# Kernel optimization log

Measured on AMD Instinct MI355X. Metric: run time of the kernel, lower is better.

## Reference

```python
import jax, jax.numpy as jnp
import numpy as np

VOCAB = 32000
HID = 1024
CUTOFFS = [0, 10000, 20000, 32000]
N_CLUSTERS = 2
DIV = 4
PROJ_DIMS = [HID // DIV**i for i in range(N_CLUSTERS + 1)]  # [1024, 256, 64]
# Faithful to source quirk: n_vocabs = cutoffs[i] + cutoffs[i+1]
LOGIT_DIMS = [CUTOFFS[i] + CUTOFFS[i + 1] for i in range(N_CLUSTERS + 1)]  # [10000, 30000, 52000]


def setup_inputs() -> dict:
    key = jax.random.key(0)
    ks = jax.random.split(key, 16)
    N = 2048
    inp = {
        "x": jax.random.normal(ks[0], (N, HID), dtype=jnp.float32),
        "y": jax.random.randint(ks[1], (N,), 0, VOCAB, dtype=jnp.int64),
    }
    s = 0.02
    # projections: Linear(hidden, proj_dims[i], bias=False); stored as [in, out]
    inp["Wp0"] = jax.random.normal(ks[2], (HID, PROJ_DIMS[0]), dtype=jnp.float32) * s
    inp["Wp1"] = jax.random.normal(ks[3], (HID, PROJ_DIMS[1]), dtype=jnp.float32) * s
    inp["Wp2"] = jax.random.normal(ks[4], (HID, PROJ_DIMS[2]), dtype=jnp.float32) * s
    # logits: Linear(proj_dims[i], LOGIT_DIMS[i]) with bias
    inp["Wl0"] = jax.random.normal(ks[5], (PROJ_DIMS[0], LOGIT_DIMS[0]), dtype=jnp.float32) * s
    inp["bl0"] = jnp.zeros((LOGIT_DIMS[0],), dtype=jnp.float32)
    inp["Wl1"] = jax.random.normal(ks[6], (PROJ_DIMS[1], LOGIT_DIMS[1]), dtype=jnp.float32) * s
    inp["bl1"] = jnp.zeros((LOGIT_DIMS[1],), dtype=jnp.float32)
    inp["Wl2"] = jax.random.normal(ks[7], (PROJ_DIMS[2], LOGIT_DIMS[2]), dtype=jnp.float32) * s
    inp["bl2"] = jnp.zeros((LOGIT_DIMS[2],), dtype=jnp.float32)
    # cluster_logit: Linear(hidden, n_clusters)
    inp["Wc"] = jax.random.normal(ks[8], (HID, N_CLUSTERS), dtype=jnp.float32) * s
    inp["bc"] = jnp.zeros((N_CLUSTERS,), dtype=jnp.float32)
    return inp


def reference(x, y, Wp0, Wp1, Wp2, Wl0, bl0, Wl1, bl1, Wl2, bl2, Wc, bc):
    # head: project (dim-preserving here) then head-vocab logits + cluster logits
    head_proj = x @ Wp0                                   # [N, 1024]
    head_logit = jnp.concatenate(
        [head_proj @ Wl0 + bl0, head_proj @ Wc + bc], axis=1
    )                                                     # [N, 10000 + 2]
    head_lp = jax.nn.log_softmax(head_logit, axis=1)

    nll = jnp.zeros(y.shape, dtype=x.dtype)

    # cluster 0: targets in [0, cutoffs[1])
    m0 = (y >= CUTOFFS[0]) & (y < CUTOFFS[1])
    t0 = jnp.clip(y - CUTOFFS[0], 0, head_lp.shape[1] - 1)
    lp0 = jnp.take_along_axis(head_lp, t0[:, None], axis=1)[:, 0]
    nll = jnp.where(m0, -lp0, nll)

    # tail clusters: small projection GEMM + log_softmax + gather, combined via masks
    tails = [(Wp1, Wl1, bl1), (Wp2, Wl2, bl2)]
    for i, (Wp, Wl, bl) in enumerate(tails, start=1):
        l, r = CUTOFFS[i], CUTOFFS[i + 1]
        mask = (y >= l) & (y < r)
        t = jnp.clip(y - l, 0, Wl.shape[1] - 1)
        tail_lp = jax.nn.log_softmax((x @ Wp) @ Wl + bl, axis=1)  # [N, LOGIT_DIMS[i]]
        # faithful to source: head column -i (reversed cluster order quirk)
        lp = head_lp[:, -i] + jnp.take_along_axis(tail_lp, t[:, None], axis=1)[:, 0]
        nll = jnp.where(mask, -lp, nll)

    return nll
```

## Files before the change

kernel.cpp:

```cpp
#include <hip/hip_runtime.h>
#include <math.h>

#define HID 1024
#define NROWS 2048

typedef __attribute__((ext_vector_type(8))) short short8;
typedef __attribute__((ext_vector_type(4))) short short4_t;
typedef __attribute__((ext_vector_type(4))) float f32x4;

__device__ __forceinline__ short f2bf(float f) {
  union { float f; unsigned u; } v; v.f = f;
  unsigned r = v.u + 0x7fffu + ((v.u >> 16) & 1u);
  return (short)(r >> 16);
}
__device__ __forceinline__ float bf2f(short s) {
  union { unsigned u; float f; } v; v.u = ((unsigned)(unsigned short)s) << 16;
  return v.f;
}
__device__ __forceinline__ float wave_sum(float a) {
#pragma unroll
  for (int off = 32; off; off >>= 1) a += __shfl_xor(a, off, 64);
  return a;
}

__global__ __launch_bounds__(256) void prep(
    const float* __restrict__ x, const int* __restrict__ y,
    const float* __restrict__ Wp0, const float* __restrict__ Wp1,
    const float* __restrict__ Wp2, const float* __restrict__ Wl0,
    const float* __restrict__ Wl1, const float* __restrict__ Wl2,
    short* __restrict__ xb,
    int* __restrict__ counts, int* __restrict__ slot_of_row,
    int* __restrict__ rows1, int* __restrict__ rows2,
    short* __restrict__ T0, short* __restrict__ T1, short* __restrict__ T2,
    short* __restrict__ T3, short* __restrict__ T4, short* __restrict__ T5) {
  const int tid = threadIdx.x;
  int b = blockIdx.x;
  if (b == 0) {
    __shared__ int c1s, c2s;
    if (tid == 0) { c1s = 0; c2s = 0; }
    __syncthreads();
    for (int r = tid; r < NROWS; r += 256) {
      const int yy = y[r];
      if (yy >= 20000) {
        const int s = atomicAdd(&c2s, 1);
        slot_of_row[r] = s; rows2[s] = r;
      } else if (yy >= 10000) {
        const int s = atomicAdd(&c1s, 1);
        slot_of_row[r] = s; rows1[s] = r;
      } else {
        slot_of_row[r] = -1;
      }
    }
    __syncthreads();
    if (tid == 0) { counts[0] = NROWS; counts[1] = c1s; counts[2] = c2s; }
    return;
  }
  if (b <= 2048) {
    const int i = ((b - 1) * 256 + tid) * 4;
    short4_t o;
    o.x = f2bf(x[i + 0]); o.y = f2bf(x[i + 1]);
    o.z = f2bf(x[i + 2]); o.w = f2bf(x[i + 3]);
    *(short4_t*)&xb[i] = o;
    return;
  }
  b -= 2049;
  const float* W; short* BT; int K, N, Npad, tn;
  if (b < 1024)                { W = Wp0; BT = T0; K = 1024; N = 1024;  Npad = 1024;  tn = 32;   }
  else if ((b -= 1024) < 256)  { W = Wp1; BT = T1; K = 1024; N = 256;   Npad = 256;   tn = 8;    }
  else if ((b -= 256) < 128)   { W = Wp2; BT = T2; K = 1024; N = 64;    Npad = 128;   tn = 4;    }
  else if ((b -= 128) < 10240) { W = Wl0; BT = T3; K = 1024; N = 10000; Npad = 10240; tn = 320;  }
  else if ((b -= 10240) < 7552){ W = Wl1; BT = T4; K = 256;  N = 30000; Npad = 30208; tn = 944;  }
  else { b -= 7552;              W = Wl2; BT = T5; K = 64;   N = 52000; Npad = 52224; tn = 1632; }

  __shared__ float T[32][33];
  const int n0 = (b % tn) * 32, k0 = (b / tn) * 32;
  const int r = tid >> 3, c = (tid & 7) * 4;
  float v0 = 0.f, v1 = 0.f, v2 = 0.f, v3 = 0.f;
  const float* p = &W[(size_t)(k0 + r) * N];
  if (n0 + c + 3 < N) {
    v0 = p[n0 + c]; v1 = p[n0 + c + 1]; v2 = p[n0 + c + 2]; v3 = p[n0 + c + 3];
  } else {
    if (n0 + c + 0 < N) v0 = p[n0 + c + 0];
    if (n0 + c + 1 < N) v1 = p[n0 + c + 1];
    if (n0 + c + 2 < N) v2 = p[n0 + c + 2];
  }
  T[r][c] = v0; T[r][c + 1] = v1; T[r][c + 2] = v2; T[r][c + 3] = v3;
  __syncthreads();
  const int nl = tid >> 3, kl = (tid & 7) * 4;
  const int n = n0 + nl;
  if (n < Npad) {
    short4_t o;
    o.x = (n < N) ? f2bf(T[kl + 0][nl]) : (short)0;
    o.y = (n < N) ? f2bf(T[kl + 1][nl]) : (short)0;
    o.z = (n < N) ? f2bf(T[kl + 2][nl]) : (short)0;
    o.w = (n < N) ? f2bf(T[kl + 3][nl]) : (short)0;
    *(short4_t*)&BT[(size_t)n * K + k0 + kl] = o;
  }
}

#define GLOAD_LDS(g, l)                                                      \
  __builtin_amdgcn_global_load_lds(                                          \
      (const __attribute__((address_space(1))) void*)(g),                    \
      (__attribute__((address_space(3))) void*)(l), 16, 0, 0)

#define BARR do { asm volatile("" ::: "memory");                             \
                  __builtin_amdgcn_s_barrier();                              \
                  asm volatile("" ::: "memory"); } while (0)

#define VMW(n) asm volatile("s_waitcnt vmcnt(" #n ")" ::: "memory")

__device__ __forceinline__ void stage_half(const short* __restrict__ src,
                                           size_t row0, int kOff, short* dst,
                                           int stride, int w, int rsub, int kc) {
  const short* g0 = src + (row0 + (size_t)(w * 8 + rsub)) * (size_t)stride
                    + kOff + kc * 8;
  GLOAD_LDS(g0, dst + w * 512);
  GLOAD_LDS(g0 + (size_t)64 * stride, dst + 4096 + w * 512);
}

#define RD_A8(dst, base) do {                                                \
  _Pragma("unroll") for (int mt = 0; mt < 4; ++mt)                           \
  _Pragma("unroll") for (int kk = 0; kk < 2; ++kk)                           \
    dst[mt * 2 + kk] = *(const short8*)((base) +                             \
        (pm * 64 + mt * 16 + ln) * 64 + (((kk * 4 + quad) ^ l7) << 3));      \
} while (0)

#define RD_B4(dst, base) do {                                                \
  _Pragma("unroll") for (int nt = 0; nt < 2; ++nt)                           \
  _Pragma("unroll") for (int kk = 0; kk < 2; ++kk)                           \
    dst[nt * 2 + kk] = *(const short8*)((base) +                             \
        (pn * 32 + nt * 16 + ln) * 64 + (((kk * 4 + quad) ^ l7) << 3));      \
} while (0)

#define MFMA16(ACC, ar, br) do {                                             \
  __builtin_amdgcn_s_setprio(1);                                             \
  _Pragma("unroll") for (int mt = 0; mt < 4; ++mt)                           \
  _Pragma("unroll") for (int nt = 0; nt < 2; ++nt)                           \
  _Pragma("unroll") for (int kk = 0; kk < 2; ++kk)                           \
    ACC[mt][nt] = __builtin_amdgcn_mfma_f32_16x16x32_bf16(                   \
        ar[mt * 2 + kk], br[nt * 2 + kk], ACC[mt][nt], 0, 0, 0);             \
  __builtin_amdgcn_s_setprio(0);                                             \
} while (0)

__device__ __forceinline__ void gemm256(
    const short* __restrict__ A, const short* __restrict__ BT,
    int K, int NT, size_t rowA0, size_t rowB0, short* lds,
    f32x4 acc[2][2][4][2], int w, int lane) {
  const int quad = lane >> 4, ln = lane & 15, l7 = lane & 7;
  const int pm = w >> 2, pn = w & 3;
  const int rsub = lane >> 3, kc = (lane & 7) ^ rsub;
  short* const Abase = lds;
  short* const Bbase = lds + 32768;

  stage_half(A,  rowA0,       0, Abase,        K, w, rsub, kc);
  stage_half(BT, rowB0,       0, Bbase,        K, w, rsub, kc);
  stage_half(BT, rowB0 + 128, 0, Bbase + 8192, K, w, rsub, kc);
  stage_half(A,  rowA0 + 128, 0, Abase + 8192, K, w, rsub, kc);

  for (int u = 0; u < NT; ++u) {
    const int c = u & 1;
    const short* Ah = Abase + c * 16384;
    const short* Bh = Bbase + c * 16384;
    short* const An = Abase + (c ^ 1) * 16384;
    short* const Bn = Bbase + (c ^ 1) * 16384;
    const int k1 = (u + 1) << 6;
    const bool more = (u < NT - 1);
    short8 aq0[8], aq1[8], bq0[4], bq1[4];
    VMW(4);
    BARR;
    RD_A8(aq0, Ah);
    RD_B4(bq0, Bh);
    if (more) stage_half(A, rowA0, k1, An, K, w, rsub, kc);
    MFMA16(acc[0][0], aq0, bq0);
    if (more) { VMW(4); } else { VMW(2); }
    BARR;
    RD_B4(bq1, Bh + 8192);
    if (more) stage_half(BT, rowB0, k1, Bn, K, w, rsub, kc);
    MFMA16(acc[0][1], aq0, bq1);
    if (more) { VMW(4); } else { VMW(0); }
    BARR;
    RD_A8(aq1, Ah + 8192);
    if (more) stage_half(BT, rowB0 + 128, k1, Bn + 8192, K, w, rsub, kc);
    MFMA16(acc[1][1], aq1, bq1);
    BARR;
    if (more) stage_half(A, rowA0 + 128, k1, An + 8192, K, w, rsub, kc);
    MFMA16(acc[1][0], aq1, bq0);
  }
}


__device__ __forceinline__ void exp_epilogue(
    f32x4 acc[2][2][4][2], const float* __restrict__ bias,
    float* __restrict__ ps, size_t c0, int Ncols, int nsplit, int r0,
    short* lds, int tid, int w, int lane) {
  const int quad = lane >> 4, ln = lane & 15;
  const int pm = w >> 2, pn = w & 3;
  float bv[2][2];
#pragma unroll
  for (int qb = 0; qb < 2; ++qb)
#pragma unroll
    for (int nt = 0; nt < 2; ++nt) {
      const size_t cg = c0 + qb * 128 + pn * 32 + nt * 16 + ln;
      bv[qb][nt] = (cg < (size_t)Ncols) ? bias[cg] : -1.0e30f;
    }
  float* const psF = (float*)lds;
  BARR;
#pragma unroll
  for (int qa = 0; qa < 2; ++qa)
#pragma unroll
    for (int qb = 0; qb < 2; ++qb)
#pragma unroll
      for (int mt = 0; mt < 4; ++mt)
#pragma unroll
        for (int r = 0; r < 4; ++r) {
          float s = __expf(acc[qa][qb][mt][0][r] + bv[qb][0]) +
                    __expf(acc[qa][qb][mt][1][r] + bv[qb][1]);
#pragma unroll
          for (int off = 1; off < 16; off <<= 1) s += __shfl_xor(s, off, 64);
          if (ln == 0)
            psF[(pn * 2 + qb) * 256 + qa * 128 + pm * 64 + mt * 16 + quad * 4 + r] = s;
        }
  BARR;
  {
    const int qb = tid >> 8, row = tid & 255;
    const int cs = (int)(c0 >> 7) + qb;
    if (cs < nsplit)
      ps[(size_t)(r0 + row) * nsplit + cs] =
          psF[(0 * 2 + qb) * 256 + row] + psF[(1 * 2 + qb) * 256 + row] +
          psF[(2 * 2 + qb) * 256 + row] + psF[(3 * 2 + qb) * 256 + row];
  }
}

__device__ __forceinline__ void mfma_mainloop(const short* aB[4], const short* bB[4],
                                              short* As, short* Bs,
                                              f32x4 acc[4][4],
                                              int K, int w, int lane) {
  const int quad = lane >> 4, ln = lane & 15;
  const int wm = w >> 1, wn = w & 1;
  const int l7 = ln & 7;
  for (int kt = 0; kt < K; kt += 64) {
#pragma unroll
    for (int i = 0; i < 4; ++i) {
      const int row = w * 32 + i * 8;
      __builtin_amdgcn_global_load_lds(
          (const __attribute__((address_space(1))) void*)(aB[i] + kt),
          (__attribute__((address_space(3))) void*)(As + row * 64), 16, 0, 0);
      __builtin_amdgcn_global_load_lds(
          (const __attribute__((address_space(1))) void*)(bB[i] + kt),
          (__attribute__((address_space(3))) void*)(Bs + row * 64), 16, 0, 0);
    }
    __syncthreads();
#pragma unroll
    for (int ks = 0; ks < 2; ++ks) {
      const int kcs = ks * 4 + quad;
      short8 af[4], bfr[4];
#pragma unroll
      for (int mt = 0; mt < 4; ++mt) {
        const int row = wm * 64 + mt * 16 + ln;
        af[mt] = *(const short8*)(As + ((row * 8 + (kcs ^ l7)) << 3));
      }
#pragma unroll
      for (int nt = 0; nt < 4; ++nt) {
        const int rowb = wn * 64 + nt * 16 + ln;
        bfr[nt] = *(const short8*)(Bs + ((rowb * 8 + (kcs ^ l7)) << 3));
      }
#pragma unroll
      for (int mt = 0; mt < 4; ++mt)
#pragma unroll
        for (int nt = 0; nt < 4; ++nt)
          acc[mt][nt] = __builtin_amdgcn_mfma_f32_16x16x32_bf16(
              af[mt], bfr[nt], acc[mt][nt], 0, 0, 0);
    }
    __syncthreads();
  }
}

__global__ __launch_bounds__(256) void proj_all(
    const short* __restrict__ xb,
    const short* __restrict__ WpT0, const short* __restrict__ WpT1,
    const short* __restrict__ WpT2,
    short* __restrict__ P0b, short* __restrict__ P1c, short* __restrict__ P2c,
    const int* __restrict__ rows1, const int* __restrict__ rows2,
    const int* __restrict__ counts) {
  int b = blockIdx.x;
  const short* BT; short* C; int N, r0, c0, cnt;
  const int* rowlist = nullptr;
  if (b < 128) {
    BT = WpT0; C = P0b; N = 1024;
    c0 = (b & 7) * 128; r0 = (b >> 3) * 128; cnt = NROWS;
  } else if (b < 160) {
    b -= 128; BT = WpT1; C = P1c; N = 256;
    c0 = (b & 1) * 128; r0 = (b >> 1) * 128; rowlist = rows1; cnt = counts[1];
  } else {
    b -= 160; BT = WpT2; C = P2c; N = 64;
    c0 = 0; r0 = b * 128; rowlist = rows2; cnt = counts[2];
  }
  if (r0 >= cnt) return;

  __shared__ short As[128 * 64];
  __shared__ short Bs[128 * 64];
  const int tid = threadIdx.x;
  const int w = tid >> 6, lane = tid & 63;
  const int quad = lane >> 4, ln = lane & 15;
  const int wm = w >> 1, wn = w & 1;
  const int rsub = lane >> 3;
  const int kc = (lane & 7) ^ rsub;
  const int K = 1024;

  const short* aB[4]; const short* bB[4];
#pragma unroll
  for (int i = 0; i < 4; ++i) {
    const int sl = r0 + w * 32 + i * 8 + rsub;
    const int ar = rowlist ? rowlist[sl < cnt ? sl : cnt - 1] : sl;
    aB[i] = xb + (size_t)ar * K + kc * 8;
    bB[i] = BT + (size_t)(c0 + w * 32 + i * 8 + rsub) * K + kc * 8;
  }

  f32x4 acc[4][4];
  const f32x4 zero = {0.f, 0.f, 0.f, 0.f};
#pragma unroll
  for (int i = 0; i < 4; ++i)
#pragma unroll
    for (int j = 0; j < 4; ++j) acc[i][j] = zero;
  mfma_mainloop(aB, bB, As, Bs, acc, K, w, lane);
#pragma unroll
  for (int mt = 0; mt < 4; ++mt)
#pragma unroll
    for (int r = 0; r < 4; ++r) {
      const int grow = r0 + wm * 64 + mt * 16 + quad * 4 + r;
#pragma unroll
      for (int nt = 0; nt < 4; ++nt) {
        const int cg = c0 + wn * 64 + nt * 16 + ln;
        if (cg < N) C[(size_t)grow * N + cg] = f2bf(acc[mt][nt][r]);
      }
    }
}

__global__ __launch_bounds__(512, 2) void logit_fused(
    const short* __restrict__ P0b, const short* __restrict__ WlT0,
    const float* __restrict__ bl0, float* __restrict__ psh,
    const short* __restrict__ P1c, const short* __restrict__ WlT1,
    const float* __restrict__ bl1, float* __restrict__ ps1,
    const short* __restrict__ P2c, const short* __restrict__ WlT2,
    const float* __restrict__ bl2, float* __restrict__ ps2,
    const int* __restrict__ counts) {
  __shared__ short lds[65536];
  const int tid = threadIdx.x;
  const int w = tid >> 6, lane = tid & 63;
  const int b = blockIdx.x;

  const short* A; const short* BT; const float* bias; float* ps;
  int K, NT, Ncols, nsplit, r0; size_t c0;
  if (b < 320) {
    const int xcd = b & 7, j = b >> 3;
    const int cb = xcd * 5 + j % 5, rb = j / 5;
    r0 = rb * 256; c0 = (size_t)cb * 256;
    A = P0b; BT = WlT0; bias = bl0; ps = psh;
    K = 1024; NT = 16; Ncols = 10000; nsplit = 79;
  } else if (b < 1264) {
    const int b1 = b - 320;
    const int rb = b1 / 118, cb = b1 % 118;
    r0 = rb * 256;
    if (r0 >= counts[1]) return;
    c0 = (size_t)cb * 256;
    A = P1c; BT = WlT1; bias = bl1; ps = ps1;
    K = 256; NT = 4; Ncols = 30000; nsplit = 235;
  } else {
    const int b2 = b - 1264;
    const int rb = b2 / 204, cb = b2 % 204;
    r0 = rb * 256;
    if (r0 >= counts[2]) return;
    c0 = (size_t)cb * 256;
    A = P2c; BT = WlT2; bias = bl2; ps = ps2;
    K = 64; NT = 1; Ncols = 52000; nsplit = 407;
  }

  f32x4 acc[2][2][4][2];
  const f32x4 zero = {0.f, 0.f, 0.f, 0.f};
#pragma unroll
  for (int qa = 0; qa < 2; ++qa)
#pragma unroll
    for (int qb = 0; qb < 2; ++qb)
#pragma unroll
      for (int mt = 0; mt < 4; ++mt)
#pragma unroll
        for (int nt = 0; nt < 2; ++nt) acc[qa][qb][mt][nt] = zero;

  gemm256(A, BT, K, NT, (size_t)r0, c0, lds, acc, w, lane);
  exp_epilogue(acc, bias, ps, c0, Ncols, nsplit, r0, lds, tid, w, lane);
}

__global__ __launch_bounds__(256) void finalize(
    const short* __restrict__ P0b, const short* __restrict__ P1c,
    const short* __restrict__ P2c,
    const short* __restrict__ WlT0, const float* __restrict__ bl0,
    const short* __restrict__ WlT1, const float* __restrict__ bl1,
    const short* __restrict__ WlT2, const float* __restrict__ bl2,
    const float* __restrict__ Wc, const float* __restrict__ bc,
    const int* __restrict__ y, const int* __restrict__ slot_of_row,
    const float* __restrict__ psh, const float* __restrict__ ps1,
    const float* __restrict__ ps2, float* __restrict__ out) {
  const int lane = threadIdx.x & 63;
  const int row = blockIdx.x * 4 + (threadIdx.x >> 6);

  float a0 = 0.f, a1 = 0.f;
  for (int k = lane; k < HID; k += 64) {
    const float p = bf2f(P0b[(size_t)row * HID + k]);
    a0 += p * Wc[2 * k];
    a1 += p * Wc[2 * k + 1];
  }
  a0 = wave_sum(a0);
  a1 = wave_sum(a1);
  const float cl0 = a0 + bc[0], cl1 = a1 + bc[1];

  float S = 0.f;
  for (int i = lane; i < 79; i += 64) S += psh[(size_t)row * 79 + i];
  S = wave_sum(S) + __expf(cl0) + __expf(cl1);
  const float lse = logf(S);

  const int yy = y[row];
  float nll;
  if (yy < 10000) {
    const short* pr = P0b + (size_t)row * 1024;
    const short* wr = WlT0 + (size_t)yy * 1024;
    float a = 0.f;
    for (int kk = lane * 4; kk < 1024; kk += 256) {
      const short4_t p = *(const short4_t*)(pr + kk);
      const short4_t wv = *(const short4_t*)(wr + kk);
      a += bf2f(p.x) * bf2f(wv.x) + bf2f(p.y) * bf2f(wv.y)
         + bf2f(p.z) * bf2f(wv.z) + bf2f(p.w) * bf2f(wv.w);
    }
    a = wave_sum(a);
    nll = -((a + bl0[yy]) - lse);
  } else if (yy < 20000) {
    const int t = yy - 10000;
    const int slot = slot_of_row[row];
    float S1 = 0.f;
    for (int i = lane; i < 235; i += 64) S1 += ps1[(size_t)slot * 235 + i];
    S1 = wave_sum(S1);
    const short* pr = P1c + (size_t)slot * 256;
    const short* wr = WlT1 + (size_t)t * 256;
    const int kk = lane * 4;
    const short4_t p = *(const short4_t*)(pr + kk);
    const short4_t wv = *(const short4_t*)(wr + kk);
    float a = bf2f(p.x) * bf2f(wv.x) + bf2f(p.y) * bf2f(wv.y)
            + bf2f(p.z) * bf2f(wv.z) + bf2f(p.w) * bf2f(wv.w);
    a = wave_sum(a);
    nll = -((cl1 - lse) + ((a + bl1[t]) - logf(S1)));
  } else {
    const int t = yy - 20000;
    const int slot = slot_of_row[row];
    float S2 = 0.f;
    for (int i = lane; i < 407; i += 64) S2 += ps2[(size_t)slot * 407 + i];
    S2 = wave_sum(S2);
    float a = 0.f;
    if (lane < 16) {
      const short* pr = P2c + (size_t)slot * 64;
      const short* wr = WlT2 + (size_t)t * 64;
      const int kk = lane * 4;
      const short4_t p = *(const short4_t*)(pr + kk);
      const short4_t wv = *(const short4_t*)(wr + kk);
      a = bf2f(p.x) * bf2f(wv.x) + bf2f(p.y) * bf2f(wv.y)
        + bf2f(p.z) * bf2f(wv.z) + bf2f(p.w) * bf2f(wv.w);
    }
    a = wave_sum(a);
    nll = -((cl0 - lse) + ((a + bl2[t]) - logf(S2)));
  }
  if (lane == 0) out[row] = nll;
}

extern "C" void kernel_launch(void* const* d_in, const int* in_sizes, int n_in,
                              void* d_out, int out_size, void* d_ws, size_t ws_size,
                              hipStream_t stream) {
  const float* x   = (const float*)d_in[0];
  const int*   y   = (const int*)d_in[1];
  const float* Wp0 = (const float*)d_in[2];
  const float* Wp1 = (const float*)d_in[3];
  const float* Wp2 = (const float*)d_in[4];
  const float* Wl0 = (const float*)d_in[5];
  const float* bl0 = (const float*)d_in[6];
  const float* Wl1 = (const float*)d_in[7];
  const float* bl1 = (const float*)d_in[8];
  const float* Wl2 = (const float*)d_in[9];
  const float* bl2 = (const float*)d_in[10];
  const float* Wc  = (const float*)d_in[11];
  const float* bc  = (const float*)d_in[12];
  float* out = (float*)d_out;

  float* fws = (float*)d_ws;
  float* psh = fws; fws += (size_t)NROWS * 79;
  float* ps1 = fws; fws += (size_t)NROWS * 235;
  float* ps2 = fws; fws += (size_t)NROWS * 407;
  int* iws = (int*)fws;
  int* counts      = iws; iws += 4;
  int* slot_of_row = iws; iws += NROWS;
  int* rows1       = iws; iws += NROWS;
  int* rows2       = iws; iws += NROWS;
  short* sp = (short*)iws;
  short* xb   = sp; sp += (size_t)NROWS * 1024;
  short* P0b  = sp; sp += (size_t)NROWS * 1024;
  short* P1c  = sp; sp += (size_t)NROWS * 256;
  short* P2c  = sp; sp += (size_t)NROWS * 64;
  short* WpT0 = sp; sp += (size_t)1024 * 1024;
  short* WpT1 = sp; sp += (size_t)256 * 1024;
  short* WpT2 = sp; sp += (size_t)128 * 1024;
  short* WlT0 = sp; sp += (size_t)10240 * 1024;
  short* WlT1 = sp; sp += (size_t)30208 * 256;
  short* WlT2 = sp; sp += (size_t)52224 * 64;

  dim3 blk(256);
  prep<<<dim3(24513), blk, 0, stream>>>(x, y, Wp0, Wp1, Wp2, Wl0, Wl1, Wl2,
                                        xb, counts, slot_of_row, rows1, rows2,
                                        WpT0, WpT1, WpT2, WlT0, WlT1, WlT2);
  proj_all<<<dim3(176), blk, 0, stream>>>(xb, WpT0, WpT1, WpT2, P0b, P1c, P2c,
                                          rows1, rows2, counts);
  logit_fused<<<dim3(2896), dim3(512), 0, stream>>>(
      P0b, WlT0, bl0, psh, P1c, WlT1, bl1, ps1, P2c, WlT2, bl2, ps2, counts);
  finalize<<<dim3(NROWS / 4), blk, 0, stream>>>(
      P0b, P1c, P2c, WlT0, bl0, WlT1, bl1, WlT2, bl2, Wc, bc, y, slot_of_row,
      psh, ps1, ps2, out);
}
```

Before: 318.3 us.

## Widen prep transpose tiles and restructure logit GEMM into 8-phase pipeline

The prep kernel now handles 64x64 transpose tiles with float4 loads and short8 stores, and converts x in 4096-element chunks per block, which cuts the block count about fourfold. The logit GEMM mainloop becomes an explicit 8-phase schedule. It prefetches two K-steps up front, adds barriers and lgkmcnt waits around each MFMA group, and takes a separate single-K-step path. The aim is cheaper weight conversion and better overlap of global-to-LDS loads with MFMA. The extra barriers could add synchronisation overhead in the GEMM.

```diff
diff --git a/kernel.cpp b/kernel.cpp
--- a/kernel.cpp
+++ b/kernel.cpp
@@ -55,46 +55,59 @@
     if (tid == 0) { counts[0] = NROWS; counts[1] = c1s; counts[2] = c2s; }
     return;
   }
-  if (b <= 2048) {
-    const int i = ((b - 1) * 256 + tid) * 4;
-    short4_t o;
-    o.x = f2bf(x[i + 0]); o.y = f2bf(x[i + 1]);
-    o.z = f2bf(x[i + 2]); o.w = f2bf(x[i + 3]);
-    *(short4_t*)&xb[i] = o;
+  if (b <= 512) {
+    const int base = (b - 1) * 4096;
+#pragma unroll
+    for (int j = 0; j < 4; ++j) {
+      const int i = base + j * 1024 + tid * 4;
+      const float4 v = *(const float4*)&x[i];
+      short4_t o;
+      o.x = f2bf(v.x); o.y = f2bf(v.y); o.z = f2bf(v.z); o.w = f2bf(v.w);
+      *(short4_t*)&xb[i] = o;
+    }
     return;
   }
-  b -= 2049;
+  b -= 513;
   const float* W; short* BT; int K, N, Npad, tn;
-  if (b < 1024)                { W = Wp0; BT = T0; K = 1024; N = 1024;  Npad = 1024;  tn = 32;   }
-  else if ((b -= 1024) < 256)  { W = Wp1; BT = T1; K = 1024; N = 256;   Npad = 256;   tn = 8;    }
-  else if ((b -= 256) < 128)   { W = Wp2; BT = T2; K = 1024; N = 64;    Npad = 128;   tn = 4;    }
-  else if ((b -= 128) < 10240) { W = Wl0; BT = T3; K = 1024; N = 10000; Npad = 10240; tn = 320;  }
-  else if ((b -= 10240) < 7552){ W = Wl1; BT = T4; K = 256;  N = 30000; Npad = 30208; tn = 944;  }
-  else { b -= 7552;              W = Wl2; BT = T5; K = 64;   N = 52000; Npad = 52224; tn = 1632; }
-
-  __shared__ float T[32][33];
-  const int n0 = (b % tn) * 32, k0 = (b / tn) * 32;
-  const int r = tid >> 3, c = (tid & 7) * 4;
-  float v0 = 0.f, v1 = 0.f, v2 = 0.f, v3 = 0.f;
-  const float* p = &W[(size_t)(k0 + r) * N];
-  if (n0 + c + 3 < N) {
-    v0 = p[n0 + c]; v1 = p[n0 + c + 1]; v2 = p[n0 + c + 2]; v3 = p[n0 + c + 3];
-  } else {
-    if (n0 + c + 0 < N) v0 = p[n0 + c + 0];
-    if (n0 + c + 1 < N) v1 = p[n0 + c + 1];
-    if (n0 + c + 2 < N) v2 = p[n0 + c + 2];
-  }
-  T[r][c] = v0; T[r][c + 1] = v1; T[r][c + 2] = v2; T[r][c + 3] = v3;
+  if (b < 256)               { W = Wp0; BT = T0; K = 1024; N = 1024;  Npad = 1024;  tn = 16;  }
+  else if ((b -= 256) < 64)  { W = Wp1; BT = T1; K = 1024; N = 256;   Npad = 256;   tn = 4;   }
+  else if ((b -= 64) < 32)   { W = Wp2; BT = T2; K = 1024; N = 64;    Npad = 128;   tn = 2;   }
+  else if ((b -= 32) < 2560) { W = Wl0; BT = T3; K = 1024; N = 10000; Npad = 10240; tn = 160; }
+  else if ((b -= 2560) < 1888){W = Wl1; BT = T4; K = 256;  N = 30000; Npad = 30208; tn = 472; }
+  else { b -= 1888;            W = Wl2; BT = T5; K = 64;   N = 52000; Npad = 52224; tn = 816; }
+
+  __shared__ float T[64][65];
+  const int n0 = (b % tn) * 64, k0 = (b / tn) * 64;
+  const int rr = tid >> 4, cc = (tid & 15) * 4;
+#pragma unroll
+  for (int j = 0; j < 4; ++j) {
+    const int kr = rr + j * 16;
+    const float* p = &W[(size_t)(k0 + kr) * N + n0 + cc];
+    float v0 = 0.f, v1 = 0.f, v2 = 0.f, v3 = 0.f;
+    if (n0 + cc + 3 < N) {
+      const float4 v = *(const float4*)p;
+      v0 = v.x; v1 = v.y; v2 = v.z; v3 = v.w;
+    } else {
+      if (n0 + cc + 0 < N) v0 = p[0];
+      if (n0 + cc + 1 < N) v1 = p[1];
+      if (n0 + cc + 2 < N) v2 = p[2];
+    }
+    T[kr][cc] = v0; T[kr][cc + 1] = v1; T[kr][cc + 2] = v2; T[kr][cc + 3] = v3;
+  }
   __syncthreads();
-  const int nl = tid >> 3, kl = (tid & 7) * 4;
+  const int nl = tid >> 2, ks = (tid & 3) * 16;
   const int n = n0 + nl;
   if (n < Npad) {
-    short4_t o;
-    o.x = (n < N) ? f2bf(T[kl + 0][nl]) : (short)0;
-    o.y = (n < N) ? f2bf(T[kl + 1][nl]) : (short)0;
-    o.z = (n < N) ? f2bf(T[kl + 2][nl]) : (short)0;
-    o.w = (n < N) ? f2bf(T[kl + 3][nl]) : (short)0;
-    *(short4_t*)&BT[(size_t)n * K + k0 + kl] = o;
+    const bool z = (n >= N);
+    short* dst = &BT[(size_t)n * K + k0 + ks];
+#pragma unroll
+    for (int h = 0; h < 2; ++h) {
+      short8 o;
+#pragma unroll
+      for (int e = 0; e < 8; ++e)
+        o[e] = z ? (short)0 : f2bf(T[ks + h * 8 + e][nl]);
+      *(short8*)(dst + h * 8) = o;
+    }
   }
 }
 
@@ -108,6 +121,9 @@
                   asm volatile("" ::: "memory"); } while (0)
 
 #define VMW(n) asm volatile("s_waitcnt vmcnt(" #n ")" ::: "memory")
+
+#define LGKM0 do { asm volatile("s_waitcnt lgkmcnt(0)" ::: "memory");        \
+                   __builtin_amdgcn_sched_barrier(0); } while (0)
 
 __device__ __forceinline__ void stage_half(const short* __restrict__ src,
                                            size_t row0, int kOff, short* dst,
@@ -142,49 +158,83 @@
   __builtin_amdgcn_s_setprio(0);                                             \
 } while (0)
 
-__device__ __forceinline__ void gemm256(
+__device__ __forceinline__ void gemm256_8ph(
     const short* __restrict__ A, const short* __restrict__ BT,
     int K, int NT, size_t rowA0, size_t rowB0, short* lds,
     f32x4 acc[2][2][4][2], int w, int lane) {
   const int quad = lane >> 4, ln = lane & 15, l7 = lane & 7;
   const int pm = w >> 2, pn = w & 3;
   const int rsub = lane >> 3, kc = (lane & 7) ^ rsub;
-  short* const Abase = lds;
-  short* const Bbase = lds + 32768;
-
-  stage_half(A,  rowA0,       0, Abase,        K, w, rsub, kc);
-  stage_half(BT, rowB0,       0, Bbase,        K, w, rsub, kc);
-  stage_half(BT, rowB0 + 128, 0, Bbase + 8192, K, w, rsub, kc);
-  stage_half(A,  rowA0 + 128, 0, Abase + 8192, K, w, rsub, kc);
-
-  for (int u = 0; u < NT; ++u) {
-    const int c = u & 1;
-    const short* Ah = Abase + c * 16384;
-    const short* Bh = Bbase + c * 16384;
-    short* const An = Abase + (c ^ 1) * 16384;
-    short* const Bn = Bbase + (c ^ 1) * 16384;
-    const int k1 = (u + 1) << 6;
-    const bool more = (u < NT - 1);
+  short* const Ab0 = lds;
+  short* const Ab1 = lds + 16384;
+  short* const Bb0 = lds + 32768;
+  short* const Bb1 = lds + 49152;
+
+  if (NT == 1) {
+    stage_half(A,  rowA0,       0, Ab0,        K, w, rsub, kc);
+    stage_half(BT, rowB0,       0, Bb0,        K, w, rsub, kc);
+    stage_half(BT, rowB0 + 128, 0, Bb0 + 8192, K, w, rsub, kc);
+    stage_half(A,  rowA0 + 128, 0, Ab0 + 8192, K, w, rsub, kc);
+    VMW(0);
+    BARR;
     short8 aq0[8], aq1[8], bq0[4], bq1[4];
-    VMW(4);
-    BARR;
-    RD_A8(aq0, Ah);
-    RD_B4(bq0, Bh);
-    if (more) stage_half(A, rowA0, k1, An, K, w, rsub, kc);
-    MFMA16(acc[0][0], aq0, bq0);
-    if (more) { VMW(4); } else { VMW(2); }
-    BARR;
-    RD_B4(bq1, Bh + 8192);
-    if (more) stage_half(BT, rowB0, k1, Bn, K, w, rsub, kc);
-    MFMA16(acc[0][1], aq0, bq1);
-    if (more) { VMW(4); } else { VMW(0); }
-    BARR;
-    RD_A8(aq1, Ah + 8192);
-    if (more) stage_half(BT, rowB0 + 128, k1, Bn + 8192, K, w, rsub, kc);
-    MFMA16(acc[1][1], aq1, bq1);
-    BARR;
-    if (more) stage_half(A, rowA0 + 128, k1, An + 8192, K, w, rsub, kc);
+    RD_A8(aq0, Ab0); RD_B4(bq0, Bb0);
+    BARR; LGKM0; MFMA16(acc[0][0], aq0, bq0); BARR;
+    RD_B4(bq1, Bb0 + 8192);
+    BARR; LGKM0; MFMA16(acc[0][1], aq0, bq1); BARR;
+    RD_A8(aq1, Ab0 + 8192);
+    BARR; LGKM0; MFMA16(acc[1][1], aq1, bq1); BARR;
     MFMA16(acc[1][0], aq1, bq0);
+    return;
+  }
+
+  stage_half(A,  rowA0,       0,  Ab0,        K, w, rsub, kc);
+  stage_half(BT, rowB0,       0,  Bb0,        K, w, rsub, kc);
+  stage_half(BT, rowB0 + 128, 0,  Bb0 + 8192, K, w, rsub, kc);
+  stage_half(A,  rowA0 + 128, 0,  Ab0 + 8192, K, w, rsub, kc);
+  stage_half(A,  rowA0,       64, Ab1,        K, w, rsub, kc);
+  stage_half(BT, rowB0,       64, Bb1,        K, w, rsub, kc);
+  stage_half(BT, rowB0 + 128, 64, Bb1 + 8192, K, w, rsub, kc);
+  stage_half(A,  rowA0 + 128, 64, Ab1 + 8192, K, w, rsub, kc);
+  VMW(8);
+  BARR;
+
+  const int NI = NT >> 1;
+  for (int i = 0; i < NI; ++i) {
+    const int t0 = 2 * i;
+    const bool more = (t0 + 2 < NT);
+    const int ku0 = (t0 + 2) << 6, ku1 = (t0 + 3) << 6;
+    short8 aq0[8], aq1[8], bq0[4], bq1[4];
+    RD_A8(aq0, Ab0); RD_B4(bq0, Bb0);
+    BARR; LGKM0; MFMA16(acc[0][0], aq0, bq0); BARR;
+    RD_B4(bq1, Bb0 + 8192);
+    if (more) stage_half(A, rowA0, ku0, Ab0, K, w, rsub, kc);
+    BARR; LGKM0; MFMA16(acc[0][1], aq0, bq1); BARR;
+    RD_A8(aq1, Ab0 + 8192);
+    if (more) stage_half(BT, rowB0, ku0, Bb0, K, w, rsub, kc);
+    BARR; LGKM0; MFMA16(acc[1][1], aq1, bq1); BARR;
+    if (more) {
+      stage_half(BT, rowB0 + 128, ku0, Bb0 + 8192, K, w, rsub, kc);
+      stage_half(A,  rowA0 + 128, ku0, Ab0 + 8192, K, w, rsub, kc);
+      VMW(8);
+    } else {
+      VMW(0);
+    }
+    BARR; MFMA16(acc[1][0], aq1, bq0); BARR;
+    RD_A8(aq0, Ab1); RD_B4(bq0, Bb1);
+    BARR; LGKM0; MFMA16(acc[0][0], aq0, bq0); BARR;
+    RD_B4(bq1, Bb1 + 8192);
+    if (more) stage_half(A, rowA0, ku1, Ab1, K, w, rsub, kc);
+    BARR; LGKM0; MFMA16(acc[0][1], aq0, bq1); BARR;
+    RD_A8(aq1, Ab1 + 8192);
+    if (more) stage_half(BT, rowB0, ku1, Bb1, K, w, rsub, kc);
+    BARR; LGKM0; MFMA16(acc[1][1], aq1, bq1); BARR;
+    if (more) {
+      stage_half(BT, rowB0 + 128, ku1, Bb1 + 8192, K, w, rsub, kc);
+      stage_half(A,  rowA0 + 128, ku1, Ab1 + 8192, K, w, rsub, kc);
+      VMW(8);
+    }
+    BARR; MFMA16(acc[1][0], aq1, bq0); BARR;
   }
 }
 
@@ -386,7 +436,7 @@
 #pragma unroll
         for (int nt = 0; nt < 2; ++nt) acc[qa][qb][mt][nt] = zero;
 
-  gemm256(A, BT, K, NT, (size_t)r0, c0, lds, acc, w, lane);
+  gemm256_8ph(A, BT, K, NT, (size_t)r0, c0, lds, acc, w, lane);
   exp_epilogue(acc, bias, ps, c0, Ncols, nsplit, r0, lds, tid, w, lane);
 }
 
@@ -509,9 +559,9 @@
   short* WlT2 = sp; sp += (size_t)52224 * 64;
 
   dim3 blk(256);
-  prep<<<dim3(24513), blk, 0, stream>>>(x, y, Wp0, Wp1, Wp2, Wl0, Wl1, Wl2,
-                                        xb, counts, slot_of_row, rows1, rows2,
-                                        WpT0, WpT1, WpT2, WlT0, WlT1, WlT2);
+  prep<<<dim3(6129), blk, 0, stream>>>(x, y, Wp0, Wp1, Wp2, Wl0, Wl1, Wl2,
+                                       xb, counts, slot_of_row, rows1, rows2,
+                                       WpT0, WpT1, WpT2, WlT0, WlT1, WlT2);
   proj_all<<<dim3(176), blk, 0, stream>>>(xb, WpT0, WpT1, WpT2, P0b, P1c, P2c,
                                           rows1, rows2, counts);
   logit_fused<<<dim3(2896), dim3(512), 0, stream>>>(
```

New measurement: 322.3 us. About the same (+1.3%).
